# Performance work log

Hardware: AMD Instinct MI355X
Metric: run time of the kernel (lower is better)

The kernel has to match this reference:

```python
import jax, jax.numpy as jnp
import numpy as np

EMBED_DIM = 512
NUM_HEADS = 8
HEAD_DIM = EMBED_DIM // NUM_HEADS
B, S = 4, 2048


def setup_inputs() -> dict:
    key = jax.random.key(0)
    ks = jax.random.split(key, 11)
    sc = 1.0 / np.sqrt(EMBED_DIM)
    return {
        "query": jax.random.normal(ks[0], (B, S, EMBED_DIM), jnp.float32),
        "key": jax.random.normal(ks[1], (B, S, EMBED_DIM), jnp.float32),
        "value": jax.random.normal(ks[2], (B, S, EMBED_DIM), jnp.float32),
        "Wq": jax.random.normal(ks[3], (EMBED_DIM, EMBED_DIM), jnp.float32) * sc,
        "bq": jnp.zeros((EMBED_DIM,), jnp.float32),
        "Wk": jax.random.normal(ks[4], (EMBED_DIM, EMBED_DIM), jnp.float32) * sc,
        "bk": jnp.zeros((EMBED_DIM,), jnp.float32),
        "Wv": jax.random.normal(ks[5], (EMBED_DIM, EMBED_DIM), jnp.float32) * sc,
        "bv": jnp.zeros((EMBED_DIM,), jnp.float32),
        "Wo": jax.random.normal(ks[6], (EMBED_DIM, EMBED_DIM), jnp.float32) * sc,
        "bo": jnp.zeros((EMBED_DIM,), jnp.float32),
    }


def reference(query, key, value, Wq, bq, Wk, bk, Wv, bv, Wo, bo):
    b = query.shape[0]
    # project and split heads: [B,S,E] -> [B,H,S,D]
    def split_heads(x):
        return x.reshape(b, -1, NUM_HEADS, HEAD_DIM).transpose(0, 2, 1, 3)

    q = split_heads(query @ Wq + bq)
    k = split_heads(key @ Wk + bk)
    v = split_heads(value @ Wv + bv)

    scores = jnp.einsum("bhqd,bhkd->bhqk", q, k) / jnp.sqrt(
        jnp.asarray(HEAD_DIM, q.dtype)
    )
    attn = jax.nn.softmax(scores, axis=-1)  # dropout = identity in eval
    context = jnp.einsum("bhqk,bhkd->bhqd", attn, v)
    context = context.transpose(0, 2, 1, 3).reshape(b, -1, EMBED_DIM)
    output = context @ Wo + bo
    return output, attn
```

## Files before the change

### kernel.cpp

```cpp
#include <hip/hip_runtime.h>
#include <cstdint>
#include <cstddef>

typedef __bf16 bf16;
typedef __bf16 bf16x8 __attribute__((ext_vector_type(8)));
typedef __bf16 bf16x4 __attribute__((ext_vector_type(4)));
typedef float  f32x4  __attribute__((ext_vector_type(4)));

#define WAITV asm volatile("s_waitcnt vmcnt(0)" ::: "memory")

__device__ __forceinline__ void gload16(const void* g, void* l) {
  __builtin_amdgcn_global_load_lds(
      (const __attribute__((address_space(1))) void*)g,
      (__attribute__((address_space(3))) void*)l, 16, 0, 0);
}

__global__ __launch_bounds__(256) void convert_x(
    const float* __restrict__ a, const float* __restrict__ b,
    const float* __restrict__ c, bf16* __restrict__ dst) {
  int i = blockIdx.x * 256 + threadIdx.x;
  const float* src = (i < 1048576) ? a : ((i < 2097152) ? b : c);
  int j = i & 1048575;
  float4 v = ((const float4*)src)[j];
  bf16x4 o;
  o.x = (bf16)v.x; o.y = (bf16)v.y; o.z = (bf16)v.z; o.w = (bf16)v.w;
  ((bf16x4*)dst)[i] = o;
}

__global__ __launch_bounds__(256) void convert_w(
    const float* __restrict__ w0, const float* __restrict__ w1,
    const float* __restrict__ w2, const float* __restrict__ w3,
    bf16* __restrict__ dst) {
  int i = blockIdx.x * 256 + threadIdx.x;
  int w = i >> 18, r = i & 262143;
  int kin = r >> 9, n = r & 511;
  const float* W = (w == 0) ? w0 : (w == 1) ? w1 : (w == 2) ? w2 : w3;
  dst[(w << 18) + (n << 9) + kin] = (bf16)W[r];
}

#define MODE_Q 0
#define MODE_K 1
#define MODE_V 2
#define MODE_O 3

template <int MODE>
__global__ __launch_bounds__(256, 2) void gemm512(
    const bf16* __restrict__ X, const bf16* __restrict__ WT,
    const float* __restrict__ bias, void* __restrict__ outp, float scale) {
  __shared__ __align__(16) bf16 As[128 * 64];
  __shared__ __align__(16) bf16 Bs[128 * 64];
  const int t = threadIdx.x, wid = t >> 6, lane = t & 63, quad = lane >> 4, l15 = lane & 15;
  const int bm = blockIdx.x, bn = blockIdx.y;
  const int wm = wid & 1, wn = wid >> 1;
  f32x4 acc[4][4] = {};
  const bf16* Ab = X + (size_t)bm * 128 * 512;
  const bf16* Bb = WT + (size_t)bn * 128 * 512;
  for (int kk = 0; kk < 8; ++kk) {
    __syncthreads();
#pragma unroll
    for (int i = 0; i < 4; ++i) {
      int seg = i * 256 + t;
      int row = seg >> 3, s = seg & 7;
      int soff = ((s ^ (row & 7)) << 3);
      gload16(Ab + row * 512 + kk * 64 + soff, (char*)As + i * 4096 + wid * 1024);
      gload16(Bb + row * 512 + kk * 64 + soff, (char*)Bs + i * 4096 + wid * 1024);
    }
    WAITV;
    __syncthreads();
#pragma unroll
    for (int k2 = 0; k2 < 2; ++k2) {
      bf16x8 af[4], bfr[4];
#pragma unroll
      for (int mi = 0; mi < 4; ++mi) {
        int arow = wm * 64 + mi * 16 + l15;
        af[mi] = *(const bf16x8*)&As[arow * 64 + (((k2 * 4 + quad) ^ (arow & 7)) << 3)];
      }
#pragma unroll
      for (int ni = 0; ni < 4; ++ni) {
        int brow = wn * 64 + ni * 16 + l15;
        bfr[ni] = *(const bf16x8*)&Bs[brow * 64 + (((k2 * 4 + quad) ^ (brow & 7)) << 3)];
      }
#pragma unroll
      for (int mi = 0; mi < 4; ++mi)
#pragma unroll
        for (int ni = 0; ni < 4; ++ni)
          acc[mi][ni] = __builtin_amdgcn_mfma_f32_16x16x32_bf16(af[mi], bfr[ni], acc[mi][ni], 0, 0, 0);
    }
  }
#pragma unroll
  for (int mi = 0; mi < 4; ++mi) {
#pragma unroll
    for (int ni = 0; ni < 4; ++ni) {
      int C = bn * 128 + wn * 64 + ni * 16 + l15;
      float bia = bias[C];
#pragma unroll
      for (int r = 0; r < 4; ++r) {
        int R = bm * 128 + wm * 64 + mi * 16 + quad * 4 + r;
        float val = acc[mi][ni][r] + bia;
        if (MODE == MODE_O) {
          ((float*)outp)[(size_t)R * 512 + C] = val;
        } else if (MODE == MODE_V) {
          int b = R >> 11, s = R & 2047, h = C >> 6, d = C & 63;
          ((bf16*)outp)[((size_t)((b * 8 + h) * 64 + d)) * 2048 + s] = (bf16)val;
        } else {
          int b = R >> 11, s = R & 2047, h = C >> 6, d = C & 63;
          ((bf16*)outp)[((size_t)((b * 8 + h) * 2048 + s)) * 64 + d] = (bf16)(val * scale);
        }
      }
    }
  }
}

__global__ __launch_bounds__(256, 4) void attn_fused(
    const bf16* __restrict__ Q, const bf16* __restrict__ K,
    const bf16* __restrict__ VT, float* __restrict__ attn,
    bf16* __restrict__ ctx_out) {
  __shared__ __align__(16) bf16 Qs[64 * 64];
  __shared__ __align__(16) bf16 Ks[64 * 64];
  __shared__ __align__(16) bf16 Vs[64 * 64];
  __shared__ __align__(16) bf16 Ps[64 * 72];
  const int t = threadIdx.x, wid = t >> 6, lane = t & 63, quad = lane >> 4, l15 = lane & 15;
  const int qt = blockIdx.x, bh = blockIdx.y;
  const bf16* Qg = Q + ((size_t)bh * 2048 + qt * 64) * 64;
  const bf16* Kg = K + (size_t)bh * 2048 * 64;
  const bf16* Vg = VT + (size_t)bh * 64 * 2048;
  float* Ag = attn + ((size_t)bh * 2048 + qt * 64) * 2048;

#pragma unroll
  for (int i = 0; i < 2; ++i) {
    int seg = i * 256 + t;
    int r = seg >> 3, s = seg & 7;
    gload16(Qg + r * 64 + ((s ^ (r & 7)) << 3), (char*)Qs + i * 4096 + wid * 1024);
  }
  WAITV;
  __syncthreads();
  bf16x8 aq[2];
  const int qrow = wid * 16 + l15;
#pragma unroll
  for (int ks = 0; ks < 2; ++ks)
    aq[ks] = *(const bf16x8*)&Qs[qrow * 64 + (((ks * 4 + quad) ^ (qrow & 7)) << 3)];

  float lsum[4] = {0.f, 0.f, 0.f, 0.f};

#pragma unroll 1
  for (int kc = 0; kc < 32; ++kc) {
    __syncthreads();
#pragma unroll
    for (int i = 0; i < 2; ++i) {
      int seg = i * 256 + t;
      int r = seg >> 3, s = seg & 7;
      gload16(Kg + ((size_t)(kc * 64 + r)) * 64 + ((s ^ (r & 7)) << 3),
              (char*)Ks + i * 4096 + wid * 1024);
    }
    WAITV;
    __syncthreads();
    f32x4 c[4];
#pragma unroll
    for (int ni = 0; ni < 4; ++ni) {
      c[ni] = (f32x4){0.f, 0.f, 0.f, 0.f};
      const int krow = ni * 16 + l15;
#pragma unroll
      for (int ks = 0; ks < 2; ++ks) {
        bf16x8 bk = *(const bf16x8*)&Ks[krow * 64 + (((ks * 4 + quad) ^ (krow & 7)) << 3)];
        c[ni] = __builtin_amdgcn_mfma_f32_16x16x32_bf16(aq[ks], bk, c[ni], 0, 0, 0);
      }
    }
#pragma unroll
    for (int r = 0; r < 4; ++r) {
      lsum[r] += __builtin_amdgcn_exp2f(c[0][r]) + __builtin_amdgcn_exp2f(c[1][r]) +
                 __builtin_amdgcn_exp2f(c[2][r]) + __builtin_amdgcn_exp2f(c[3][r]);
    }
  }
  float il[4];
#pragma unroll
  for (int r = 0; r < 4; ++r) {
    float sum = lsum[r];
    sum += __shfl_xor(sum, 1);
    sum += __shfl_xor(sum, 2);
    sum += __shfl_xor(sum, 4);
    sum += __shfl_xor(sum, 8);
    il[r] = 1.0f / sum;
  }

  f32x4 o[4] = {};
#pragma unroll 1
  for (int kc = 0; kc < 32; ++kc) {
    __syncthreads();
#pragma unroll
    for (int i = 0; i < 2; ++i) {
      int seg = i * 256 + t;
      int r = seg >> 3, s = seg & 7;
      gload16(Kg + ((size_t)(kc * 64 + r)) * 64 + ((s ^ (r & 7)) << 3),
              (char*)Ks + i * 4096 + wid * 1024);
      gload16(Vg + ((size_t)r) * 2048 + kc * 64 + ((s ^ (r & 7)) << 3),
              (char*)Vs + i * 4096 + wid * 1024);
    }
    WAITV;
    __syncthreads();
    f32x4 c[4];
#pragma unroll
    for (int ni = 0; ni < 4; ++ni) {
      c[ni] = (f32x4){0.f, 0.f, 0.f, 0.f};
      const int krow = ni * 16 + l15;
#pragma unroll
      for (int ks = 0; ks < 2; ++ks) {
        bf16x8 bk = *(const bf16x8*)&Ks[krow * 64 + (((ks * 4 + quad) ^ (krow & 7)) << 3)];
        c[ni] = __builtin_amdgcn_mfma_f32_16x16x32_bf16(aq[ks], bk, c[ni], 0, 0, 0);
      }
    }
#pragma unroll
    for (int ni = 0; ni < 4; ++ni) {
#pragma unroll
      for (int r = 0; r < 4; ++r) {
        float p = __builtin_amdgcn_exp2f(c[ni][r]) * il[r];
        Ag[(size_t)(wid * 16 + quad * 4 + r) * 2048 + kc * 64 + ni * 16 + l15] = p;
        Ps[(wid * 16 + quad * 4 + r) * 72 + ni * 16 + l15] = (bf16)p;
      }
    }
    bf16x8 pa[2];
#pragma unroll
    for (int ks = 0; ks < 2; ++ks)
      pa[ks] = *(const bf16x8*)&Ps[(wid * 16 + l15) * 72 + ks * 32 + quad * 8];
#pragma unroll
    for (int ni = 0; ni < 4; ++ni) {
      const int vrow = ni * 16 + l15;
#pragma unroll
      for (int ks = 0; ks < 2; ++ks) {
        bf16x8 bv = *(const bf16x8*)&Vs[vrow * 64 + (((ks * 4 + quad) ^ (vrow & 7)) << 3)];
        o[ni] = __builtin_amdgcn_mfma_f32_16x16x32_bf16(pa[ks], bv, o[ni], 0, 0, 0);
      }
    }
  }

  const int b = bh >> 3, h = bh & 7;
#pragma unroll
  for (int ni = 0; ni < 4; ++ni) {
#pragma unroll
    for (int r = 0; r < 4; ++r) {
      int s = qt * 64 + wid * 16 + quad * 4 + r;
      ctx_out[((size_t)(b * 2048 + s)) * 512 + h * 64 + ni * 16 + l15] = (bf16)o[ni][r];
    }
  }
}

extern "C" void kernel_launch(void* const* d_in, const int* in_sizes, int n_in,
                              void* d_out, int out_size, void* d_ws, size_t ws_size,
                              hipStream_t stream) {
  const float* query = (const float*)d_in[0];
  const float* key   = (const float*)d_in[1];
  const float* value = (const float*)d_in[2];
  const float* Wq = (const float*)d_in[3];
  const float* bq = (const float*)d_in[4];
  const float* Wk = (const float*)d_in[5];
  const float* bk = (const float*)d_in[6];
  const float* Wv = (const float*)d_in[7];
  const float* bv = (const float*)d_in[8];
  const float* Wo = (const float*)d_in[9];
  const float* bo = (const float*)d_in[10];

  float* out  = (float*)d_out;
  float* attn = out + (size_t)4 * 2048 * 512;

  char* ws = (char*)d_ws;
  bf16* Xqkv = (bf16*)ws;
  bf16* WT   = (bf16*)(ws + 25165824);
  bf16* qb   = (bf16*)(ws + 27262976);
  bf16* kb   = (bf16*)(ws + 35651584);
  bf16* vtb  = (bf16*)(ws + 44040192);
  bf16* ctx  = (bf16*)ws;

  convert_x<<<12288, 256, 0, stream>>>(query, key, value, Xqkv);
  convert_w<<<4096, 256, 0, stream>>>(Wq, Wk, Wv, Wo, WT);

  dim3 g(64, 4);
  const float QSCALE = 0.18033688011112042592f;
  gemm512<MODE_Q><<<g, 256, 0, stream>>>(Xqkv,           WT,          bq, qb,  QSCALE);
  gemm512<MODE_K><<<g, 256, 0, stream>>>(Xqkv + 4194304, WT + 262144, bk, kb,  1.0f);
  gemm512<MODE_V><<<g, 256, 0, stream>>>(Xqkv + 8388608, WT + 524288, bv, vtb, 1.0f);

  attn_fused<<<dim3(32, 32), 256, 0, stream>>>(qb, kb, vtb, attn, ctx);

  gemm512<MODE_O><<<g, 256, 0, stream>>>(ctx, WT + 786432, bo, out, 1.0f);
}
```

Before: 723.4 us.

## Double-buffer LDS tiles in GEMM and attention with prefetch and vmcnt waits

Adds double-buffered shared-memory staging to the projection GEMM and both attention passes, prefetching the next K/V (and A/B) tile while computing on the current one, with partial vmcnt waits in place of full drains. The attention kernel also remaps block indices to group heads for cache locality, writes the attention matrix with nontemporal stores, and switches the P tile to an XOR-swizzled layout. This is meant to hide global load latency and cut LDS bank conflicts, at the cost of more LDS per block (possibly lower occupancy) and fragile hand-counted waitcnt values, since the global stores to attn also count toward vmcnt.

```diff
diff --git a/kernel.cpp b/kernel.cpp
--- a/kernel.cpp
+++ b/kernel.cpp
@@ -7,7 +7,8 @@
 typedef __bf16 bf16x4 __attribute__((ext_vector_type(4)));
 typedef float  f32x4  __attribute__((ext_vector_type(4)));
 
-#define WAITV asm volatile("s_waitcnt vmcnt(0)" ::: "memory")
+#define BAR() do { asm volatile("" ::: "memory"); __builtin_amdgcn_s_barrier(); asm volatile("" ::: "memory"); } while (0)
+#define WAIT_VM(N) asm volatile("s_waitcnt vmcnt(" #N ")" ::: "memory")
 
 __device__ __forceinline__ void gload16(const void* g, void* l) {
   __builtin_amdgcn_global_load_lds(
@@ -47,38 +48,46 @@
 __global__ __launch_bounds__(256, 2) void gemm512(
     const bf16* __restrict__ X, const bf16* __restrict__ WT,
     const float* __restrict__ bias, void* __restrict__ outp, float scale) {
-  __shared__ __align__(16) bf16 As[128 * 64];
-  __shared__ __align__(16) bf16 Bs[128 * 64];
+  __shared__ __align__(16) bf16 As[2][128 * 64];
+  __shared__ __align__(16) bf16 Bs[2][128 * 64];
   const int t = threadIdx.x, wid = t >> 6, lane = t & 63, quad = lane >> 4, l15 = lane & 15;
   const int bm = blockIdx.x, bn = blockIdx.y;
   const int wm = wid & 1, wn = wid >> 1;
   f32x4 acc[4][4] = {};
   const bf16* Ab = X + (size_t)bm * 128 * 512;
   const bf16* Bb = WT + (size_t)bn * 128 * 512;
-  for (int kk = 0; kk < 8; ++kk) {
-    __syncthreads();
+
+  auto stage = [&](int kk, int p) {
 #pragma unroll
     for (int i = 0; i < 4; ++i) {
       int seg = i * 256 + t;
       int row = seg >> 3, s = seg & 7;
       int soff = ((s ^ (row & 7)) << 3);
-      gload16(Ab + row * 512 + kk * 64 + soff, (char*)As + i * 4096 + wid * 1024);
-      gload16(Bb + row * 512 + kk * 64 + soff, (char*)Bs + i * 4096 + wid * 1024);
-    }
-    WAITV;
-    __syncthreads();
+      gload16(Ab + row * 512 + kk * 64 + soff, (char*)As[p] + i * 4096 + wid * 1024);
+      gload16(Bb + row * 512 + kk * 64 + soff, (char*)Bs[p] + i * 4096 + wid * 1024);
+    }
+  };
+
+  stage(0, 0);
+  for (int kk = 0; kk < 8; ++kk) {
+    BAR();
+    if (kk < 7) stage(kk + 1, (kk + 1) & 1);
+    if (kk < 7) { WAIT_VM(8); } else { WAIT_VM(0); }
+    BAR();
+    const bf16* Ap = As[kk & 1];
+    const bf16* Bp = Bs[kk & 1];
 #pragma unroll
     for (int k2 = 0; k2 < 2; ++k2) {
       bf16x8 af[4], bfr[4];
 #pragma unroll
       for (int mi = 0; mi < 4; ++mi) {
         int arow = wm * 64 + mi * 16 + l15;
-        af[mi] = *(const bf16x8*)&As[arow * 64 + (((k2 * 4 + quad) ^ (arow & 7)) << 3)];
+        af[mi] = *(const bf16x8*)&Ap[arow * 64 + (((k2 * 4 + quad) ^ (arow & 7)) << 3)];
       }
 #pragma unroll
       for (int ni = 0; ni < 4; ++ni) {
         int brow = wn * 64 + ni * 16 + l15;
-        bfr[ni] = *(const bf16x8*)&Bs[brow * 64 + (((k2 * 4 + quad) ^ (brow & 7)) << 3)];
+        bfr[ni] = *(const bf16x8*)&Bp[brow * 64 + (((k2 * 4 + quad) ^ (brow & 7)) << 3)];
       }
 #pragma unroll
       for (int mi = 0; mi < 4; ++mi)
@@ -115,45 +124,62 @@
     const bf16* __restrict__ Q, const bf16* __restrict__ K,
     const bf16* __restrict__ VT, float* __restrict__ attn,
     bf16* __restrict__ ctx_out) {
-  __shared__ __align__(16) bf16 Qs[64 * 64];
-  __shared__ __align__(16) bf16 Ks[64 * 64];
-  __shared__ __align__(16) bf16 Vs[64 * 64];
-  __shared__ __align__(16) bf16 Ps[64 * 72];
+  __shared__ __align__(16) bf16 KAb[64 * 64];
+  __shared__ __align__(16) bf16 KBb[64 * 64];
+  __shared__ __align__(16) bf16 VAb[64 * 64];
+  __shared__ __align__(16) bf16 VBb[64 * 64];
+  __shared__ __align__(16) bf16 Ps[64 * 64];
   const int t = threadIdx.x, wid = t >> 6, lane = t & 63, quad = lane >> 4, l15 = lane & 15;
-  const int qt = blockIdx.x, bh = blockIdx.y;
+  int lin = blockIdx.x + (blockIdx.y << 5);
+  int swz = ((lin & 7) << 7) + (lin >> 3);
+  const int qt = swz & 31, bh = swz >> 5;
   const bf16* Qg = Q + ((size_t)bh * 2048 + qt * 64) * 64;
   const bf16* Kg = K + (size_t)bh * 2048 * 64;
   const bf16* Vg = VT + (size_t)bh * 64 * 2048;
   float* Ag = attn + ((size_t)bh * 2048 + qt * 64) * 2048;
 
+  auto stageK = [&](int kc, bf16* buf) {
+#pragma unroll
+    for (int i = 0; i < 2; ++i) {
+      int seg = i * 256 + t, r = seg >> 3, s = seg & 7;
+      gload16(Kg + ((size_t)(kc * 64 + r)) * 64 + ((s ^ (r & 7)) << 3),
+              (char*)buf + i * 4096 + wid * 1024);
+    }
+  };
+  auto stageV = [&](int kc, bf16* buf) {
+#pragma unroll
+    for (int i = 0; i < 2; ++i) {
+      int seg = i * 256 + t, r = seg >> 3, s = seg & 7;
+      gload16(Vg + ((size_t)r) * 2048 + kc * 64 + ((s ^ (r & 7)) << 3),
+              (char*)buf + i * 4096 + wid * 1024);
+    }
+  };
+
 #pragma unroll
   for (int i = 0; i < 2; ++i) {
-    int seg = i * 256 + t;
-    int r = seg >> 3, s = seg & 7;
-    gload16(Qg + r * 64 + ((s ^ (r & 7)) << 3), (char*)Qs + i * 4096 + wid * 1024);
-  }
-  WAITV;
-  __syncthreads();
+    int seg = i * 256 + t, r = seg >> 3, s = seg & 7;
+    gload16(Qg + r * 64 + ((s ^ (r & 7)) << 3), (char*)KAb + i * 4096 + wid * 1024);
+  }
+  stageK(0, KBb);
+  WAIT_VM(2);
+  BAR();
   bf16x8 aq[2];
   const int qrow = wid * 16 + l15;
 #pragma unroll
   for (int ks = 0; ks < 2; ++ks)
-    aq[ks] = *(const bf16x8*)&Qs[qrow * 64 + (((ks * 4 + quad) ^ (qrow & 7)) << 3)];
+    aq[ks] = *(const bf16x8*)&KAb[qrow * 64 + (((ks * 4 + quad) ^ (qrow & 7)) << 3)];
+  asm volatile("s_waitcnt lgkmcnt(0)" ::: "memory");
+  __builtin_amdgcn_sched_barrier(0);
 
   float lsum[4] = {0.f, 0.f, 0.f, 0.f};
 
 #pragma unroll 1
   for (int kc = 0; kc < 32; ++kc) {
-    __syncthreads();
-#pragma unroll
-    for (int i = 0; i < 2; ++i) {
-      int seg = i * 256 + t;
-      int r = seg >> 3, s = seg & 7;
-      gload16(Kg + ((size_t)(kc * 64 + r)) * 64 + ((s ^ (r & 7)) << 3),
-              (char*)Ks + i * 4096 + wid * 1024);
-    }
-    WAITV;
-    __syncthreads();
+    BAR();
+    if (kc < 31) stageK(kc + 1, (kc & 1) ? KBb : KAb);
+    if (kc < 31) { WAIT_VM(2); } else { WAIT_VM(0); }
+    BAR();
+    const bf16* kb_ = (kc & 1) ? KAb : KBb;
     f32x4 c[4];
 #pragma unroll
     for (int ni = 0; ni < 4; ++ni) {
@@ -161,7 +187,7 @@
       const int krow = ni * 16 + l15;
 #pragma unroll
       for (int ks = 0; ks < 2; ++ks) {
-        bf16x8 bk = *(const bf16x8*)&Ks[krow * 64 + (((ks * 4 + quad) ^ (krow & 7)) << 3)];
+        bf16x8 bk = *(const bf16x8*)&kb_[krow * 64 + (((ks * 4 + quad) ^ (krow & 7)) << 3)];
         c[ni] = __builtin_amdgcn_mfma_f32_16x16x32_bf16(aq[ks], bk, c[ni], 0, 0, 0);
       }
     }
@@ -182,21 +208,22 @@
     il[r] = 1.0f / sum;
   }
 
+  stageK(0, KBb);
+  stageV(0, VBb);
   f32x4 o[4] = {};
 #pragma unroll 1
   for (int kc = 0; kc < 32; ++kc) {
-    __syncthreads();
-#pragma unroll
-    for (int i = 0; i < 2; ++i) {
-      int seg = i * 256 + t;
-      int r = seg >> 3, s = seg & 7;
-      gload16(Kg + ((size_t)(kc * 64 + r)) * 64 + ((s ^ (r & 7)) << 3),
-              (char*)Ks + i * 4096 + wid * 1024);
-      gload16(Vg + ((size_t)r) * 2048 + kc * 64 + ((s ^ (r & 7)) << 3),
-              (char*)Vs + i * 4096 + wid * 1024);
-    }
-    WAITV;
-    __syncthreads();
+    BAR();
+    if (kc < 31) {
+      stageK(kc + 1, (kc & 1) ? KBb : KAb);
+      stageV(kc + 1, (kc & 1) ? VBb : VAb);
+    }
+    if (kc == 0)      { WAIT_VM(4); }
+    else if (kc < 31) { WAIT_VM(20); }
+    else              { WAIT_VM(16); }
+    BAR();
+    const bf16* kb_ = (kc & 1) ? KAb : KBb;
+    const bf16* vb_ = (kc & 1) ? VAb : VBb;
     f32x4 c[4];
 #pragma unroll
     for (int ni = 0; ni < 4; ++ni) {
@@ -204,7 +231,7 @@
       const int krow = ni * 16 + l15;
 #pragma unroll
       for (int ks = 0; ks < 2; ++ks) {
-        bf16x8 bk = *(const bf16x8*)&Ks[krow * 64 + (((ks * 4 + quad) ^ (krow & 7)) << 3)];
+        bf16x8 bk = *(const bf16x8*)&kb_[krow * 64 + (((ks * 4 + quad) ^ (krow & 7)) << 3)];
         c[ni] = __builtin_amdgcn_mfma_f32_16x16x32_bf16(aq[ks], bk, c[ni], 0, 0, 0);
       }
     }
@@ -213,20 +240,22 @@
 #pragma unroll
       for (int r = 0; r < 4; ++r) {
         float p = __builtin_amdgcn_exp2f(c[ni][r]) * il[r];
-        Ag[(size_t)(wid * 16 + quad * 4 + r) * 2048 + kc * 64 + ni * 16 + l15] = p;
-        Ps[(wid * 16 + quad * 4 + r) * 72 + ni * 16 + l15] = (bf16)p;
+        int row = wid * 16 + quad * 4 + r;
+        __builtin_nontemporal_store(p, &Ag[(size_t)row * 2048 + kc * 64 + ni * 16 + l15]);
+        *(bf16*)((char*)Ps + row * 128 + ((((ni * 2 + (l15 >> 3)) ^ (row & 7)) << 4) + ((l15 & 7) << 1))) = (bf16)p;
       }
     }
     bf16x8 pa[2];
+    const int prow = wid * 16 + l15;
 #pragma unroll
     for (int ks = 0; ks < 2; ++ks)
-      pa[ks] = *(const bf16x8*)&Ps[(wid * 16 + l15) * 72 + ks * 32 + quad * 8];
+      pa[ks] = *(const bf16x8*)((char*)Ps + prow * 128 + (((ks * 4 + quad) ^ (prow & 7)) << 4));
 #pragma unroll
     for (int ni = 0; ni < 4; ++ni) {
       const int vrow = ni * 16 + l15;
 #pragma unroll
       for (int ks = 0; ks < 2; ++ks) {
-        bf16x8 bv = *(const bf16x8*)&Vs[vrow * 64 + (((ks * 4 + quad) ^ (vrow & 7)) << 3)];
+        bf16x8 bv = *(const bf16x8*)&vb_[vrow * 64 + (((ks * 4 + quad) ^ (vrow & 7)) << 3)];
         o[ni] = __builtin_amdgcn_mfma_f32_16x16x32_bf16(pa[ks], bv, o[ni], 0, 0, 0);
       }
     }
```

Measured after the change: 714.5 us. About the same (-1.2%).
